# Kernel tuning notes

Hardware: AMD Instinct MI355X
Metric: run time of the kernel (lower is better)

The kernel has to match this reference:

```python
import jax, jax.numpy as jnp
import numpy as np

NEG = -1e9  # stand-in for -inf in masked_fill; avoids NaN rows for never-gathered states


def _residual(x, w1, b1, w2, b2):
    # ResidualLayerOld: two relu linears with a residual connection (eval mode, no dropout)
    h = jax.nn.relu(x @ w1.T + b1)
    return x + jax.nn.relu(h @ w2.T + b2)


def setup_inputs() -> dict:
    key = jax.random.key(0)
    B, T, V, C, H, SPW = 16, 256, 32000, 1024, 512, 8
    ks = jax.random.split(key, 32)
    s = 0.05  # keep logits in a sane range
    inp = {
        'start_emb': jax.random.normal(ks[0], (C, H), jnp.float32) * s,
        'start_l1w': jax.random.normal(ks[1], (H, H), jnp.float32) * s,
        'start_l1b': jnp.zeros((H,), jnp.float32),
        'start_l2w': jax.random.normal(ks[2], (H, H), jnp.float32) * s,
        'start_l2b': jnp.zeros((H,), jnp.float32),
        'start_ow': jax.random.normal(ks[3], (1, H), jnp.float32) * s,
        'start_ob': jnp.zeros((1,), jnp.float32),
        'state_emb': jax.random.normal(ks[4], (C, H), jnp.float32) * s,
        'trans_l1w': jax.random.normal(ks[5], (H, H), jnp.float32) * s,
        'trans_l1b': jnp.zeros((H,), jnp.float32),
        'trans_l2w': jax.random.normal(ks[6], (H, H), jnp.float32) * s,
        'trans_l2b': jnp.zeros((H,), jnp.float32),
        'proj_w': jax.random.normal(ks[7], (C, H), jnp.float32) * s,
        'pret_emb': jax.random.normal(ks[8], (C, H), jnp.float32) * s,
        'term_l1w': jax.random.normal(ks[9], (H, H), jnp.float32) * s,
        'term_l1b': jnp.zeros((H,), jnp.float32),
        'term_l2w': jax.random.normal(ks[10], (H, H), jnp.float32) * s,
        'term_l2b': jnp.zeros((H,), jnp.float32),
        'term_ow': jax.random.normal(ks[11], (V, H), jnp.float32) * s,
        'term_ob': jnp.zeros((V,), jnp.float32),
        'text': jax.random.randint(ks[12], (B, T), 0, V, jnp.int32),
        'word2state': jax.random.randint(ks[13], (V, SPW), 0, C, jnp.int32),
    }
    return inp


def reference(start_emb, start_l1w, start_l1b, start_l2w, start_l2b, start_ow, start_ob,
              state_emb, trans_l1w, trans_l1b, trans_l2w, trans_l2b, proj_w,
              pret_emb, term_l1w, term_l1b, term_l2w, term_l2b, term_ow, term_ob,
              text, word2state):
    C, H = start_emb.shape
    V, SPW = word2state.shape

    # start: MLP(C,H)->(C,1) -> log_softmax over C
    start = jax.nn.log_softmax(
        (_residual(start_emb, start_l1w, start_l1b, start_l2w, start_l2b) @ start_ow.T + start_ob).squeeze(-1))

    # transition: [C,C] log_softmax over next state
    trans = jax.nn.log_softmax(
        _residual(state_emb, trans_l1w, trans_l1b, trans_l2w, trans_l2b) @ proj_w.T, axis=-1)

    # emission: [C,V] logits, masked to the sparse word->state assignment, log_softmax over V
    term_logits = _residual(pret_emb, term_l1w, term_l1b, term_l2w, term_l2b) @ term_ow.T + term_ob
    mask = jnp.zeros((C, V), bool).at[word2state.reshape(-1), jnp.repeat(jnp.arange(V), SPW)].set(True)
    emission = jax.nn.log_softmax(jnp.where(mask, term_logits, NEG), axis=-1)

    # clamp: gather per-timestep [SPW,SPW] transition blocks + emissions
    cs = word2state[text]                               # [B,T,SPW]
    pot = trans[cs[:, :-1, :, None], cs[:, 1:, None, :]]  # [B,T-1,SPW,SPW] (prev i, next j)
    init = start[cs[:, 0]]                              # [B,SPW]
    obs = emission[cs, text[:, :, None]]                # [B,T,SPW]
    pot = pot.at[:, 0].add((init + obs[:, 0])[:, :, None])
    pot = pot + obs[:, 1:][:, :, None, :]               # add obs_{t+1} along next-state j
    pot = jnp.swapaxes(pot, -1, -2)                     # [B,T-1,next,prev], as in clamp()

    # forward algorithm (fb kernel's alpha pass): alpha_{t+1}[n] = LSE_p pot[t,n,p] + alpha_t[p]
    def step(alpha, p):
        a = jax.nn.logsumexp(p + alpha[:, None, :], axis=-1)
        return a, None

    B = text.shape[0]
    alpha0 = jnp.zeros((B, SPW), pot.dtype)
    alphaT, _ = jax.lax.scan(step, alpha0, jnp.swapaxes(pot, 0, 1))
    evidence = jax.nn.logsumexp(alphaT, axis=-1).sum()  # full-length sequences
    return evidence
```

## Files before the change

### kernel.cpp

```cpp
#include <hip/hip_runtime.h>
#include <hip/hip_bf16.h>

#define C_DIM 1024
#define H_DIM 512
#define V_DIM 32000
#define B_DIM 16
#define T_DIM 256
#define SPW   8
#define NSLOT 32
#define NSEG  32

typedef unsigned short u16;
typedef unsigned int   u32;
typedef __attribute__((ext_vector_type(8))) short bf16x8;
typedef __attribute__((ext_vector_type(4))) float f32x4;

__device__ __forceinline__ u16 f2b(float f) {
    union { float f; u32 i; } x; x.f = f;
    u32 i = x.i;
    i += 0x7fffu + ((i >> 16) & 1u);
    return (u16)(i >> 16);
}
__device__ __forceinline__ float b2f(u16 u) {
    union { u32 i; float f; } x; x.i = ((u32)u) << 16; return x.f;
}
__device__ __forceinline__ float dot8_bf16(uint4 u, const float4 tw0, const float4 tw1) {
    return tw0.x * b2f((u16)(u.x & 0xffff)) + tw0.y * b2f((u16)(u.x >> 16))
         + tw0.z * b2f((u16)(u.y & 0xffff)) + tw0.w * b2f((u16)(u.y >> 16))
         + tw1.x * b2f((u16)(u.z & 0xffff)) + tw1.y * b2f((u16)(u.z >> 16))
         + tw1.z * b2f((u16)(u.w & 0xffff)) + tw1.w * b2f((u16)(u.w >> 16));
}
__device__ __forceinline__ float dot8_bf16(uint4 u, const f32x4 tw0, const f32x4 tw1) {
    return tw0[0] * b2f((u16)(u.x & 0xffff)) + tw0[1] * b2f((u16)(u.x >> 16))
         + tw0[2] * b2f((u16)(u.y & 0xffff)) + tw0[3] * b2f((u16)(u.y >> 16))
         + tw1[0] * b2f((u16)(u.z & 0xffff)) + tw1[1] * b2f((u16)(u.z >> 16))
         + tw1[2] * b2f((u16)(u.w & 0xffff)) + tw1[3] * b2f((u16)(u.w >> 16));
}

struct CvtArgs {
    const float* src[6];
    u16*         dst[6];
    int          n[6];
    float*       zero;
    int          zn;
    float*       out;
};

__global__ __launch_bounds__(256) void cvt_kern(CvtArgs a)
{
    int seg = blockIdx.y;
    if (seg == 6) {
        for (int i = blockIdx.x * 256 + threadIdx.x; i < a.zn; i += gridDim.x * 256)
            a.zero[i] = 0.0f;
        if (blockIdx.x == 0 && threadIdx.x == 0) a.out[0] = 0.0f;
        return;
    }
    const float4* s = (const float4*)a.src[seg];
    ushort4* d = (ushort4*)a.dst[seg];
    int n4 = a.n[seg] >> 2;
    for (int i = blockIdx.x * 256 + threadIdx.x; i < n4; i += gridDim.x * 256) {
        float4 v = s[i];
        ushort4 o;
        o.x = f2b(v.x); o.y = f2b(v.y); o.z = f2b(v.z); o.w = f2b(v.w);
        d[i] = o;
    }
}

struct MlpArgs {
    const u16*   A[3];
    const u16*   W[3];
    const float* bias[3];
    const float* resid[3];
    u16*         out[3];
    const float* csrc[4];
    u16*         cdst[4];
    int          cn[4];
};

__global__ __launch_bounds__(256) void mlp16_kern(MlpArgs args)
{
    if (blockIdx.z == 3) {
        int idx = (blockIdx.y * gridDim.x + blockIdx.x) * 256 + threadIdx.x;
        int stride = gridDim.x * gridDim.y * 256;
#pragma unroll
        for (int s = 0; s < 4; s++) {
            const float4* sp = (const float4*)args.csrc[s];
            ushort4* dp = (ushort4*)args.cdst[s];
            int n4 = args.cn[s] >> 2;
            for (int t = idx; t < n4; t += stride) {
                float4 v = sp[t];
                ushort4 o;
                o.x = f2b(v.x); o.y = f2b(v.y); o.z = f2b(v.z); o.w = f2b(v.w);
                dp[t] = o;
            }
        }
        return;
    }
    const int N = H_DIM, K = H_DIM;
    int z = blockIdx.z;
    const u16* A = args.A[z];
    const u16* B = args.W[z];
    const float* bias = args.bias[z];
    const float* resid = args.resid[z];
    u16* out = args.out[z];

    __shared__ __align__(16) u16 As[2][64][40];
    __shared__ __align__(16) u16 Bs[2][64][40];
    int tid  = threadIdx.x;
    int m0 = blockIdx.x * 64, n0 = blockIdx.y * 64;
    int wave = tid >> 6, lane = tid & 63;
    int wr = wave >> 1, wc = wave & 1;
    int srow = tid >> 2, scol = (tid & 3) << 3;
    int quad = lane >> 4, l16 = lane & 15;
    f32x4 acc[2][2] = {};

    const u16* ap = A + (size_t)(m0 + srow) * K + scol;
    const u16* bp = B + (size_t)(n0 + srow) * K + scol;

    *(uint4*)&As[0][srow][scol] = *(const uint4*)ap;
    *(uint4*)&Bs[0][srow][scol] = *(const uint4*)bp;
    __syncthreads();
    int cur = 0;
#pragma unroll 1
    for (int k0 = 0; k0 + 32 < K; k0 += 32) {
        uint4 an = *(const uint4*)(ap + k0 + 32);
        uint4 bn = *(const uint4*)(bp + k0 + 32);
        bf16x8 af0 = *(const bf16x8*)&As[cur][wr * 32 + l16][quad * 8];
        bf16x8 af1 = *(const bf16x8*)&As[cur][wr * 32 + 16 + l16][quad * 8];
        bf16x8 bf0 = *(const bf16x8*)&Bs[cur][wc * 32 + l16][quad * 8];
        bf16x8 bf1 = *(const bf16x8*)&Bs[cur][wc * 32 + 16 + l16][quad * 8];
        acc[0][0] = __builtin_amdgcn_mfma_f32_16x16x32_bf16(af0, bf0, acc[0][0], 0, 0, 0);
        acc[0][1] = __builtin_amdgcn_mfma_f32_16x16x32_bf16(af0, bf1, acc[0][1], 0, 0, 0);
        acc[1][0] = __builtin_amdgcn_mfma_f32_16x16x32_bf16(af1, bf0, acc[1][0], 0, 0, 0);
        acc[1][1] = __builtin_amdgcn_mfma_f32_16x16x32_bf16(af1, bf1, acc[1][1], 0, 0, 0);
        *(uint4*)&As[cur ^ 1][srow][scol] = an;
        *(uint4*)&Bs[cur ^ 1][srow][scol] = bn;
        __syncthreads();
        cur ^= 1;
    }
    {
        bf16x8 af0 = *(const bf16x8*)&As[cur][wr * 32 + l16][quad * 8];
        bf16x8 af1 = *(const bf16x8*)&As[cur][wr * 32 + 16 + l16][quad * 8];
        bf16x8 bf0 = *(const bf16x8*)&Bs[cur][wc * 32 + l16][quad * 8];
        bf16x8 bf1 = *(const bf16x8*)&Bs[cur][wc * 32 + 16 + l16][quad * 8];
        acc[0][0] = __builtin_amdgcn_mfma_f32_16x16x32_bf16(af0, bf0, acc[0][0], 0, 0, 0);
        acc[0][1] = __builtin_amdgcn_mfma_f32_16x16x32_bf16(af0, bf1, acc[0][1], 0, 0, 0);
        acc[1][0] = __builtin_amdgcn_mfma_f32_16x16x32_bf16(af1, bf0, acc[1][0], 0, 0, 0);
        acc[1][1] = __builtin_amdgcn_mfma_f32_16x16x32_bf16(af1, bf1, acc[1][1], 0, 0, 0);
    }
#pragma unroll
    for (int sm = 0; sm < 2; sm++)
#pragma unroll
        for (int sn = 0; sn < 2; sn++) {
            int n = n0 + wc * 32 + sn * 16 + l16;
            float bv = bias[n];
#pragma unroll
            for (int reg = 0; reg < 4; reg++) {
                int m = m0 + wr * 32 + sm * 16 + quad * 4 + reg;
                float v = fmaxf(acc[sm][sn][reg] + bv, 0.0f);
                if (resid) v += resid[(size_t)m * N + n];
                out[(size_t)m * N + n] = f2b(v);
            }
        }
}

__global__ __launch_bounds__(256) void fused_mid_kern(
    const u16* __restrict__ Rtrans16, const u16* __restrict__ proj16,
    float* __restrict__ TL, float* __restrict__ rowsum,
    const u16* __restrict__ Rterm16, const float* __restrict__ tow,
    const float* __restrict__ tob, const int* __restrict__ w2s,
    float* __restrict__ Zpart, float* __restrict__ Lmat,
    const u16* __restrict__ Rstart16, const float* __restrict__ sow,
    const float* __restrict__ sob, float* __restrict__ startv,
    float* __restrict__ Ssum)
{
    __shared__ __align__(16) u16 As[2][64][40];
    __shared__ __align__(16) u16 Bs[2][64][40];
    int bx = blockIdx.x;
    int tid = threadIdx.x;
    int wid = tid >> 6, lane = tid & 63;

    if (bx < 256) {
        const int K = H_DIM;
        int m0 = (bx & 15) * 64, n0 = (bx >> 4) * 64;
        int wr = wid >> 1, wc = wid & 1;
        int srow = tid >> 2, scol = (tid & 3) << 3;
        int quad = lane >> 4, l16 = lane & 15;
        f32x4 acc[2][2] = {};

        const u16* ap = Rtrans16 + (size_t)(m0 + srow) * K + scol;
        const u16* bp = proj16 + (size_t)(n0 + srow) * K + scol;

        *(uint4*)&As[0][srow][scol] = *(const uint4*)ap;
        *(uint4*)&Bs[0][srow][scol] = *(const uint4*)bp;
        __syncthreads();
        int cur = 0;
#pragma unroll 1
        for (int k0 = 0; k0 + 32 < K; k0 += 32) {
            uint4 an = *(const uint4*)(ap + k0 + 32);
            uint4 bn = *(const uint4*)(bp + k0 + 32);
            bf16x8 af0 = *(const bf16x8*)&As[cur][wr * 32 + l16][quad * 8];
            bf16x8 af1 = *(const bf16x8*)&As[cur][wr * 32 + 16 + l16][quad * 8];
            bf16x8 bf0 = *(const bf16x8*)&Bs[cur][wc * 32 + l16][quad * 8];
            bf16x8 bf1 = *(const bf16x8*)&Bs[cur][wc * 32 + 16 + l16][quad * 8];
            acc[0][0] = __builtin_amdgcn_mfma_f32_16x16x32_bf16(af0, bf0, acc[0][0], 0, 0, 0);
            acc[0][1] = __builtin_amdgcn_mfma_f32_16x16x32_bf16(af0, bf1, acc[0][1], 0, 0, 0);
            acc[1][0] = __builtin_amdgcn_mfma_f32_16x16x32_bf16(af1, bf0, acc[1][0], 0, 0, 0);
            acc[1][1] = __builtin_amdgcn_mfma_f32_16x16x32_bf16(af1, bf1, acc[1][1], 0, 0, 0);
            *(uint4*)&As[cur ^ 1][srow][scol] = an;
            *(uint4*)&Bs[cur ^ 1][srow][scol] = bn;
            __syncthreads();
            cur ^= 1;
        }
        {
            bf16x8 af0 = *(const bf16x8*)&As[cur][wr * 32 + l16][quad * 8];
            bf16x8 af1 = *(const bf16x8*)&As[cur][wr * 32 + 16 + l16][quad * 8];
            bf16x8 bf0 = *(const bf16x8*)&Bs[cur][wc * 32 + l16][quad * 8];
            bf16x8 bf1 = *(const bf16x8*)&Bs[cur][wc * 32 + 16 + l16][quad * 8];
            acc[0][0] = __builtin_amdgcn_mfma_f32_16x16x32_bf16(af0, bf0, acc[0][0], 0, 0, 0);
            acc[0][1] = __builtin_amdgcn_mfma_f32_16x16x32_bf16(af0, bf1, acc[0][1], 0, 0, 0);
            acc[1][0] = __builtin_amdgcn_mfma_f32_16x16x32_bf16(af1, bf0, acc[1][0], 0, 0, 0);
            acc[1][1] = __builtin_amdgcn_mfma_f32_16x16x32_bf16(af1, bf1, acc[1][1], 0, 0, 0);
        }
#pragma unroll
        for (int sm = 0; sm < 2; sm++)
#pragma unroll
            for (int reg = 0; reg < 4; reg++) {
                int m = m0 + wr * 32 + sm * 16 + quad * 4 + reg;
                float e = 0.0f;
#pragma unroll
                for (int sn = 0; sn < 2; sn++) {
                    int n = n0 + wc * 32 + sn * 16 + l16;
                    float v = acc[sm][sn][reg];
                    TL[(size_t)m * C_DIM + n] = v;
                    e += __expf(v);
                }
                e += __shfl_xor(e, 1, 64);
                e += __shfl_xor(e, 2, 64);
                e += __shfl_xor(e, 4, 64);
                e += __shfl_xor(e, 8, 64);
                if (l16 == 0) atomicAdd(rowsum + m, e);
            }
        return;
    }

    if (bx < 256 + V_DIM / 8) {
        int qbid = bx - 256;
        int slotid = qbid & (NSLOT - 1);
#pragma unroll
        for (int h = 0; h < 2; h++) {
            int v = (qbid * 4 + wid) * 2 + h;
            const f32x4* twp = (const f32x4*)(tow + (size_t)v * H_DIM);
            f32x4 tw0 = __builtin_nontemporal_load(&twp[lane * 2]);
            f32x4 tw1 = __builtin_nontemporal_load(&twp[lane * 2 + 1]);
            float ob = __builtin_nontemporal_load(&tob[v]);
            int cs[SPW];
#pragma unroll
            for (int s = 0; s < SPW; s++) cs[s] = w2s[v * SPW + s];
            uint4 rv[SPW];
#pragma unroll
            for (int s = 0; s < SPW; s++)
                rv[s] = ((const uint4*)(Rterm16 + (size_t)cs[s] * H_DIM))[lane];
            float d[SPW];
#pragma unroll
            for (int s = 0; s < SPW; s++) {
                d[s] = dot8_bf16(rv[s], tw0, tw1);
                d[s] += __shfl_xor(d[s], 1, 64);
                d[s] += __shfl_xor(d[s], 2, 64);
                d[s] += __shfl_xor(d[s], 4, 64);
            }
            float x = d[0];
            int myc = cs[0];
#pragma unroll
            for (int s = 1; s < SPW; s++) {
                if ((lane & 7) == s) { x = d[s]; myc = cs[s]; }
            }
            x += __shfl_xor(x, 8, 64);
            x += __shfl_xor(x, 16, 64);
            x += __shfl_xor(x, 32, 64);
            u32 dupmask = 0;
#pragma unroll
            for (int s = 1; s < SPW; s++) {
                bool dp = false;
#pragma unroll
                for (int s2 = 0; s2 < s; s2++) dp = dp || (cs[s2] == cs[s]);
                if (dp) dupmask |= (1u << s);
            }
            if (lane < 8) {
                Lmat[(size_t)v * SPW + lane] = x + ob;
                if (!((dupmask >> lane) & 1u))
                    atomicAdd(Zpart + (size_t)myc * NSLOT + slotid, __expf(x + ob));
            }
        }
        return;
    }

    int sbid = bx - (256 + V_DIM / 8);
    int c = sbid * 4 + wid;
    uint4 rv = ((const uint4*)(Rstart16 + (size_t)c * H_DIM))[lane];
    const float4* wp = (const float4*)(sow);
    float4 w0 = wp[lane * 2], w1 = wp[lane * 2 + 1];
    float d = dot8_bf16(rv, w0, w1);
    for (int off = 1; off < 64; off <<= 1) d += __shfl_xor(d, off, 64);
    if (lane == 0) {
        d += sob[0];
        startv[c] = d;
        atomicAdd(Ssum + (sbid & (NSLOT - 1)), __expf(d));
    }
}

__device__ __forceinline__ float lsm_combine(float accv, float mv, int i, int j)
{
    float x[8];
#pragma unroll
    for (int k = 0; k < 8; k++) {
        float a = __shfl(accv, k * 8 + i, 64);
        float b = __shfl(mv,  j * 8 + k, 64);
        x[k] = a + b;
    }
    float mx = fmaxf(fmaxf(fmaxf(x[0], x[1]), fmaxf(x[2], x[3])),
                     fmaxf(fmaxf(x[4], x[5]), fmaxf(x[6], x[7])));
    float s = 0.0f;
#pragma unroll
    for (int k = 0; k < 8; k++) s += __expf(x[k] - mx);
    return mx + __logf(s);
}

__global__ __launch_bounds__(256) void scanA_kern(
    const float* __restrict__ TL, const float* __restrict__ rowsum,
    const float* __restrict__ Lmat, const float* __restrict__ Zpart,
    const float* __restrict__ startv, const float* __restrict__ Ssum,
    const int* __restrict__ text, const int* __restrict__ w2s,
    float* __restrict__ Mc)
{
    __shared__ float sLZ[C_DIM];
    __shared__ float sLR[C_DIM];
    int tid = threadIdx.x;
    int wid = tid >> 6, lane = tid & 63;
    for (int c = tid; c < C_DIM; c += 256) {
        const float4* zp = (const float4*)(Zpart + (size_t)c * NSLOT);
        float4 z0 = zp[0], z1 = zp[1], z2 = zp[2], z3 = zp[3];
        float4 z4 = zp[4], z5 = zp[5], z6 = zp[6], z7 = zp[7];
        float z = ((z0.x + z0.y + z0.z + z0.w) + (z1.x + z1.y + z1.z + z1.w))
                + ((z2.x + z2.y + z2.z + z2.w) + (z3.x + z3.y + z3.z + z3.w))
                + ((z4.x + z4.y + z4.z + z4.w) + (z5.x + z5.y + z5.z + z5.w))
                + ((z6.x + z6.y + z6.z + z6.w) + (z7.x + z7.y + z7.z + z7.w));
        sLZ[c] = __logf(z);
        sLR[c] = __logf(rowsum[c]);
    }
    __syncthreads();

    int g = blockIdx.x * 4 + wid;
    int b = g >> 5, seg = g & (NSEG - 1);
    int t0 = seg * (T_DIM / NSEG);
    int cnt = min(T_DIM / NSEG, (T_DIM - 1) - t0);
    int i = lane & 7, j = lane >> 3;
    const int* txt = text + b * T_DIM;

    float logS = 0.0f;
    if (t0 == 0) {
        float ss = 0.0f;
#pragma unroll
        for (int k = 0; k < NSLOT; k++) ss += Ssum[k];
        logS = __logf(ss);
    }

    auto potval = [&](int t) -> float {
        int vt  = txt[t];
        int vt1 = txt[t + 1];
        int ci = w2s[vt * SPW + i];
        int cj = w2s[vt1 * SPW + j];
        float p = TL[(size_t)ci * C_DIM + cj] - sLR[ci]
                + Lmat[(size_t)vt1 * SPW + j] - sLZ[cj];
        if (t == 0)
            p += startv[ci] - logS + Lmat[(size_t)vt * SPW + i] - sLZ[ci];
        return p;
    };

    float acc = potval(t0);
    if (cnt > 1) {
        float nv = potval(t0 + 1);
        for (int t = t0 + 1; t < t0 + cnt; t++) {
            float nv2 = (t + 1 < t0 + cnt) ? potval(t + 1) : 0.0f;
            acc = lsm_combine(acc, nv, i, j);
            nv = nv2;
        }
    }
    Mc[(size_t)g * 64 + lane] = acc;
}

__global__ __launch_bounds__(512) void scanB_kern(const float* __restrict__ Mc,
                                                  float* __restrict__ out)
{
    __shared__ float Lb[8][64];
    int b = blockIdx.x;
    int w = threadIdx.x >> 6, lane = threadIdx.x & 63;
    int i = lane & 7, j = lane >> 3;
    const float* base = Mc + (size_t)b * NSEG * 64;

    float m0 = base[(size_t)(4 * w + 0) * 64 + lane];
    float m1 = base[(size_t)(4 * w + 1) * 64 + lane];
    float m2 = base[(size_t)(4 * w + 2) * 64 + lane];
    float m3 = base[(size_t)(4 * w + 3) * 64 + lane];
    float r01 = lsm_combine(m0, m1, i, j);
    float r23 = lsm_combine(m2, m3, i, j);
    float r = lsm_combine(r01, r23, i, j);
    Lb[w][lane] = r;
    __syncthreads();
    float a, m;
    if (w < 4) { a = Lb[2 * w][lane]; m = Lb[2 * w + 1][lane]; r = lsm_combine(a, m, i, j); }
    __syncthreads();
    if (w < 4) Lb[w][lane] = r;
    __syncthreads();
    if (w < 2) { a = Lb[2 * w][lane]; m = Lb[2 * w + 1][lane]; r = lsm_combine(a, m, i, j); }
    __syncthreads();
    if (w < 2) Lb[w][lane] = r;
    __syncthreads();
    if (w == 0) {
        a = Lb[0][lane]; m = Lb[1][lane];
        r = lsm_combine(a, m, i, j);
        float mx = r;
        for (int o = 1; o < 64; o <<= 1) mx = fmaxf(mx, __shfl_xor(mx, o, 64));
        float e = __expf(r - mx);
        for (int o = 1; o < 64; o <<= 1) e += __shfl_xor(e, o, 64);
        if (lane == 0) atomicAdd(out, mx + __logf(e));
    }
}

extern "C" void kernel_launch(void* const* d_in, const int* in_sizes, int n_in,
                              void* d_out, int out_size, void* d_ws, size_t ws_size,
                              hipStream_t stream)
{
    const float* start_emb = (const float*)d_in[0];
    const float* start_l1w = (const float*)d_in[1];
    const float* start_l1b = (const float*)d_in[2];
    const float* start_l2w = (const float*)d_in[3];
    const float* start_l2b = (const float*)d_in[4];
    const float* start_ow  = (const float*)d_in[5];
    const float* start_ob  = (const float*)d_in[6];
    const float* state_emb = (const float*)d_in[7];
    const float* trans_l1w = (const float*)d_in[8];
    const float* trans_l1b = (const float*)d_in[9];
    const float* trans_l2w = (const float*)d_in[10];
    const float* trans_l2b = (const float*)d_in[11];
    const float* proj_w    = (const float*)d_in[12];
    const float* pret_emb  = (const float*)d_in[13];
    const float* term_l1w  = (const float*)d_in[14];
    const float* term_l1b  = (const float*)d_in[15];
    const float* term_l2w  = (const float*)d_in[16];
    const float* term_l2b  = (const float*)d_in[17];
    const float* term_ow   = (const float*)d_in[18];
    const float* term_ob   = (const float*)d_in[19];
    const int*   text      = (const int*)d_in[20];
    const int*   w2s       = (const int*)d_in[21];

    char* w = (char*)d_ws;
    const u32 MB = 1u << 20;
    const size_t CH = (size_t)C_DIM * H_DIM;
    const size_t HH = (size_t)H_DIM * H_DIM;

    u16*   emb16  = (u16*)(w);
    u16*   w16    = (u16*)(w + 3u * MB);
    u16*   proj16 = (u16*)(w + 6u * MB);
    u16*   H16    = (u16*)(w + 7u * MB);
    u16*   R16    = (u16*)(w + 10u * MB);
    float* TL     = (float*)(w + 13u * MB);
    float* startv = (float*)(w + 17u * MB);
    float* Mc     = (float*)(w + 17u * MB + 4096);
    float* Zpart  = (float*)(w + 18u * MB);
    float* Ssum   = Zpart + (size_t)C_DIM * NSLOT;
    float* rowsum = Ssum + NSLOT;
    float* Lmat   = (float*)(w + 19u * MB);

    u16* semb16 = emb16;
    u16* temb16 = emb16 + CH;
    u16* pemb16 = emb16 + 2 * CH;
    u16* sl1w16 = w16;
    u16* sl2w16 = w16 + HH;
    u16* tl1w16 = w16 + 2 * HH;
    u16* tl2w16 = w16 + 3 * HH;
    u16* ml1w16 = w16 + 4 * HH;
    u16* ml2w16 = w16 + 5 * HH;
    u16* Hs = H16, *Ht = H16 + CH, *Hp = H16 + 2 * CH;
    u16* Rstart16 = R16;
    u16* Rtrans16 = R16 + CH;
    u16* Rterm16  = R16 + 2 * CH;

    dim3 blk256(256);

    CvtArgs cv;
    cv.src[0] = start_emb; cv.dst[0] = semb16; cv.n[0] = (int)CH;
    cv.src[1] = state_emb; cv.dst[1] = temb16; cv.n[1] = (int)CH;
    cv.src[2] = pret_emb;  cv.dst[2] = pemb16; cv.n[2] = (int)CH;
    cv.src[3] = start_l1w; cv.dst[3] = sl1w16; cv.n[3] = (int)HH;
    cv.src[4] = trans_l1w; cv.dst[4] = tl1w16; cv.n[4] = (int)HH;
    cv.src[5] = term_l1w;  cv.dst[5] = ml1w16; cv.n[5] = (int)HH;
    cv.zero = Zpart; cv.zn = C_DIM * NSLOT + NSLOT + C_DIM;
    cv.out = (float*)d_out;
    cvt_kern<<<dim3(64, 7), blk256, 0, stream>>>(cv);

    MlpArgs l1;
    l1.A[0] = semb16; l1.A[1] = temb16; l1.A[2] = pemb16;
    l1.W[0] = sl1w16; l1.W[1] = tl1w16; l1.W[2] = ml1w16;
    l1.bias[0] = start_l1b; l1.bias[1] = trans_l1b; l1.bias[2] = term_l1b;
    l1.resid[0] = nullptr; l1.resid[1] = nullptr; l1.resid[2] = nullptr;
    l1.out[0] = Hs; l1.out[1] = Ht; l1.out[2] = Hp;
    l1.csrc[0] = start_l2w; l1.cdst[0] = sl2w16; l1.cn[0] = (int)HH;
    l1.csrc[1] = trans_l2w; l1.cdst[1] = tl2w16; l1.cn[1] = (int)HH;
    l1.csrc[2] = term_l2w;  l1.cdst[2] = ml2w16; l1.cn[2] = (int)HH;
    l1.csrc[3] = proj_w;    l1.cdst[3] = proj16; l1.cn[3] = (int)CH;

    MlpArgs l2;
    l2.A[0] = Hs; l2.A[1] = Ht; l2.A[2] = Hp;
    l2.W[0] = sl2w16; l2.W[1] = tl2w16; l2.W[2] = ml2w16;
    l2.bias[0] = start_l2b; l2.bias[1] = trans_l2b; l2.bias[2] = term_l2b;
    l2.resid[0] = start_emb; l2.resid[1] = state_emb; l2.resid[2] = pret_emb;
    l2.out[0] = Rstart16; l2.out[1] = Rtrans16; l2.out[2] = Rterm16;
    l2.csrc[0] = nullptr; l2.cdst[0] = nullptr; l2.cn[0] = 0;
    l2.csrc[1] = nullptr; l2.cdst[1] = nullptr; l2.cn[1] = 0;
    l2.csrc[2] = nullptr; l2.cdst[2] = nullptr; l2.cn[2] = 0;
    l2.csrc[3] = nullptr; l2.cdst[3] = nullptr; l2.cn[3] = 0;

    mlp16_kern<<<dim3(16, 8, 4), blk256, 0, stream>>>(l1);
    mlp16_kern<<<dim3(16, 8, 3), blk256, 0, stream>>>(l2);

    fused_mid_kern<<<256 + V_DIM / 8 + C_DIM / 4, blk256, 0, stream>>>(
        Rtrans16, proj16, TL, rowsum,
        Rterm16, term_ow, term_ob, w2s, Zpart, Lmat,
        Rstart16, start_ow, start_ob, startv, Ssum);

    scanA_kern<<<B_DIM * NSEG / 4, blk256, 0, stream>>>(TL, rowsum, Lmat, Zpart,
                                                        startv, Ssum, text, w2s, Mc);
    scanB_kern<<<B_DIM, dim3(512), 0, stream>>>(Mc, (float*)d_out);
}
```

Measured before the change: 220.8 us.

## Fuse scan reduction into segment kernel via last-block atomic counter

Merges the two scan kernels into one. Each segment block now has a single wavefront, and the last block to finish for a batch (detected with an atomic counter that is zeroed in the conversion kernel) runs the serial 32-way log-semiring combine and adds the result to the output. This removes one kernel launch and its dependency gap, and spreads the segment work over more, smaller blocks. In exchange, each 64-thread block now recomputes the 1024-entry log tables in shared memory on its own, which is more redundant work, and the final reduction becomes a serial chain on one wave.

```diff
diff --git a/kernel.cpp b/kernel.cpp
--- a/kernel.cpp
+++ b/kernel.cpp
@@ -326,18 +326,17 @@
     return mx + __logf(s);
 }
 
-__global__ __launch_bounds__(256) void scanA_kern(
+__global__ __launch_bounds__(64) void scanAf_kern(
     const float* __restrict__ TL, const float* __restrict__ rowsum,
     const float* __restrict__ Lmat, const float* __restrict__ Zpart,
     const float* __restrict__ startv, const float* __restrict__ Ssum,
     const int* __restrict__ text, const int* __restrict__ w2s,
-    float* __restrict__ Mc)
+    float* __restrict__ Mc, u32* __restrict__ cnt, float* __restrict__ out)
 {
     __shared__ float sLZ[C_DIM];
     __shared__ float sLR[C_DIM];
-    int tid = threadIdx.x;
-    int wid = tid >> 6, lane = tid & 63;
-    for (int c = tid; c < C_DIM; c += 256) {
+    int lane = threadIdx.x;
+    for (int c = lane; c < C_DIM; c += 64) {
         const float4* zp = (const float4*)(Zpart + (size_t)c * NSLOT);
         float4 z0 = zp[0], z1 = zp[1], z2 = zp[2], z3 = zp[3];
         float4 z4 = zp[4], z5 = zp[5], z6 = zp[6], z7 = zp[7];
@@ -350,10 +349,10 @@
     }
     __syncthreads();
 
-    int g = blockIdx.x * 4 + wid;
+    int g = blockIdx.x;
     int b = g >> 5, seg = g & (NSEG - 1);
     int t0 = seg * (T_DIM / NSEG);
-    int cnt = min(T_DIM / NSEG, (T_DIM - 1) - t0);
+    int cntn = min(T_DIM / NSEG, (T_DIM - 1) - t0);
     int i = lane & 7, j = lane >> 3;
     const int* txt = text + b * T_DIM;
 
@@ -378,47 +377,29 @@
     };
 
     float acc = potval(t0);
-    if (cnt > 1) {
+    if (cntn > 1) {
         float nv = potval(t0 + 1);
-        for (int t = t0 + 1; t < t0 + cnt; t++) {
-            float nv2 = (t + 1 < t0 + cnt) ? potval(t + 1) : 0.0f;
+        for (int t = t0 + 1; t < t0 + cntn; t++) {
+            float nv2 = (t + 1 < t0 + cntn) ? potval(t + 1) : 0.0f;
             acc = lsm_combine(acc, nv, i, j);
             nv = nv2;
         }
     }
     Mc[(size_t)g * 64 + lane] = acc;
-}
-
-__global__ __launch_bounds__(512) void scanB_kern(const float* __restrict__ Mc,
-                                                  float* __restrict__ out)
-{
-    __shared__ float Lb[8][64];
-    int b = blockIdx.x;
-    int w = threadIdx.x >> 6, lane = threadIdx.x & 63;
-    int i = lane & 7, j = lane >> 3;
-    const float* base = Mc + (size_t)b * NSEG * 64;
-
-    float m0 = base[(size_t)(4 * w + 0) * 64 + lane];
-    float m1 = base[(size_t)(4 * w + 1) * 64 + lane];
-    float m2 = base[(size_t)(4 * w + 2) * 64 + lane];
-    float m3 = base[(size_t)(4 * w + 3) * 64 + lane];
-    float r01 = lsm_combine(m0, m1, i, j);
-    float r23 = lsm_combine(m2, m3, i, j);
-    float r = lsm_combine(r01, r23, i, j);
-    Lb[w][lane] = r;
-    __syncthreads();
-    float a, m;
-    if (w < 4) { a = Lb[2 * w][lane]; m = Lb[2 * w + 1][lane]; r = lsm_combine(a, m, i, j); }
-    __syncthreads();
-    if (w < 4) Lb[w][lane] = r;
-    __syncthreads();
-    if (w < 2) { a = Lb[2 * w][lane]; m = Lb[2 * w + 1][lane]; r = lsm_combine(a, m, i, j); }
-    __syncthreads();
-    if (w < 2) Lb[w][lane] = r;
-    __syncthreads();
-    if (w == 0) {
-        a = Lb[0][lane]; m = Lb[1][lane];
-        r = lsm_combine(a, m, i, j);
+
+    u32 prev = 0;
+    if (lane == 0) {
+        __threadfence();
+        prev = __hip_atomic_fetch_add(cnt + b, 1u, __ATOMIC_ACQ_REL,
+                                      __HIP_MEMORY_SCOPE_AGENT);
+    }
+    prev = (u32)__shfl((int)prev, 0, 64);
+    if (prev == (u32)(NSEG - 1)) {
+        __builtin_amdgcn_fence(__ATOMIC_ACQUIRE, "agent");
+        const float* base = Mc + (size_t)b * NSEG * 64;
+        float r = base[lane];
+        for (int s = 1; s < NSEG; s++)
+            r = lsm_combine(r, base[(size_t)s * 64 + lane], i, j);
         float mx = r;
         for (int o = 1; o < 64; o <<= 1) mx = fmaxf(mx, __shfl_xor(mx, o, 64));
         float e = __expf(r - mx);
@@ -470,6 +451,7 @@
     float* Zpart  = (float*)(w + 18u * MB);
     float* Ssum   = Zpart + (size_t)C_DIM * NSLOT;
     float* rowsum = Ssum + NSLOT;
+    u32*   bcnt   = (u32*)(rowsum + C_DIM);
     float* Lmat   = (float*)(w + 19u * MB);
 
     u16* semb16 = emb16;
@@ -495,7 +477,8 @@
     cv.src[3] = start_l1w; cv.dst[3] = sl1w16; cv.n[3] = (int)HH;
     cv.src[4] = trans_l1w; cv.dst[4] = tl1w16; cv.n[4] = (int)HH;
     cv.src[5] = term_l1w;  cv.dst[5] = ml1w16; cv.n[5] = (int)HH;
-    cv.zero = Zpart; cv.zn = C_DIM * NSLOT + NSLOT + C_DIM;
+    cv.zero = Zpart;
+    cv.zn = C_DIM * NSLOT + NSLOT + C_DIM + B_DIM;
     cv.out = (float*)d_out;
     cvt_kern<<<dim3(64, 7), blk256, 0, stream>>>(cv);
 
@@ -529,7 +512,7 @@
         Rterm16, term_ow, term_ob, w2s, Zpart, Lmat,
         Rstart16, start_ow, start_ob, startv, Ssum);
 
-    scanA_kern<<<B_DIM * NSEG / 4, blk256, 0, stream>>>(TL, rowsum, Lmat, Zpart,
-                                                        startv, Ssum, text, w2s, Mc);
-    scanB_kern<<<B_DIM, dim3(512), 0, stream>>>(Mc, (float*)d_out);
-}
+    scanAf_kern<<<B_DIM * NSEG, dim3(64), 0, stream>>>(
+        TL, rowsum, Lmat, Zpart, startv, Ssum, text, w2s,
+        Mc, bcnt, (float*)d_out);
+}
```

Result: slower. 248.2 us (+12.4%).
